# Kernel optimization log

Measured on AMD Instinct MI355X. Metric: run time of the kernel, lower is better.

Reference implementation:

```python
import jax, jax.numpy as jnp
import numpy as np
from jax import lax

IMG = 512            # image H = W
FH = FW = 32         # feature map spatial size
A = 9                # anchors per location (3 sizes x 3 ratios)
N = FH * FW * A      # total anchors = 9216
IOU_THR = 0.7
MIN_SCORE = 0.5
MIN_SIZE = 1e-3


def make_anchors():
    """Anchors in centroid format (cx, cy, w, h), ordered (H, W, A)."""
    stride = IMG / FH
    sizes = np.array([32.0, 64.0, 128.0])
    ratios = np.array([0.5, 1.0, 2.0])
    ws = (sizes[:, None] / np.sqrt(ratios)[None, :]).reshape(-1)  # (A,)
    hs = (sizes[:, None] * np.sqrt(ratios)[None, :]).reshape(-1)  # (A,)
    cx = (np.arange(FW) + 0.5) * stride
    cy = (np.arange(FH) + 0.5) * stride
    CX = np.broadcast_to(cx[None, :, None], (FH, FW, A))
    CY = np.broadcast_to(cy[:, None, None], (FH, FW, A))
    Wg = np.broadcast_to(ws[None, None, :], (FH, FW, A))
    Hg = np.broadcast_to(hs[None, None, :], (FH, FW, A))
    anc = np.stack([CX, CY, Wg, Hg], axis=-1).reshape(-1, 4)
    return jnp.asarray(anc, dtype=jnp.float32)


def pairwise_iou(b):
    # b: (N,4) corners x1,y1,x2,y2
    x1, y1, x2, y2 = b[:, 0], b[:, 1], b[:, 2], b[:, 3]
    area = (x2 - x1) * (y2 - y1)
    ix1 = jnp.maximum(x1[:, None], x1[None, :])
    iy1 = jnp.maximum(y1[:, None], y1[None, :])
    ix2 = jnp.minimum(x2[:, None], x2[None, :])
    iy2 = jnp.minimum(y2[:, None], y2[None, :])
    inter = jnp.maximum(ix2 - ix1, 0.0) * jnp.maximum(iy2 - iy1, 0.0)
    union = area[:, None] + area[None, :] - inter
    return inter / jnp.maximum(union, 1e-9)


def nms_keep(boxes, scores, valid):
    """Greedy NMS. Returns bool keep mask of shape (N,). Index decisions only."""
    s = jnp.where(valid, scores, -jnp.inf)
    order = jnp.argsort(-s)
    b = boxes[order]
    v = valid[order]
    ious = pairwise_iou(b)  # (N, N)
    idx = jnp.arange(N)

    def body(i, supp):
        keep_i = (~supp[i]) & v[i]
        return supp | (keep_i & (ious[i] > IOU_THR) & (idx > i))

    supp = lax.fori_loop(0, N, body, jnp.zeros(N, dtype=bool))
    keep_sorted = (~supp) & v
    return jnp.zeros(N, dtype=bool).at[order].set(keep_sorted)


def setup_inputs() -> dict:
    key = jax.random.key(0)
    ks = jax.random.split(key, 4)
    return {
        "feature_map": jax.random.normal(ks[0], (1, 256, FH, FW), jnp.float32),
        "conv1_w": jax.random.normal(ks[1], (512, 256, 3, 3), jnp.float32) * 0.02,
        "conv1_b": jnp.zeros((512,), jnp.float32),
        "conv2_w": jax.random.normal(ks[2], (A, 512), jnp.float32) * 0.01,
        "conv2_b": jnp.zeros((A,), jnp.float32),
        "conv3_w": jax.random.normal(ks[3], (4 * A, 512), jnp.float32) * 0.01,
        "conv3_b": jnp.zeros((4 * A,), jnp.float32),
    }


def reference(feature_map, conv1_w, conv1_b, conv2_w, conv2_b, conv3_w, conv3_b):
    anchors = make_anchors()  # (N,4) cx,cy,w,h

    # --- conv backbone head ---
    h = lax.conv_general_dilated(
        feature_map, conv1_w, (1, 1), "SAME",
        dimension_numbers=("NCHW", "OIHW", "NCHW"))
    h = jax.nn.relu(h + conv1_b[None, :, None, None])  # (1,512,H,W)

    scores = jax.nn.sigmoid(
        jnp.einsum("bchw,ac->bahw", h, conv2_w) + conv2_b[None, :, None, None])
    scores = scores.transpose(0, 2, 3, 1).reshape(-1)  # (N,) ordered (H,W,A)

    off = jnp.einsum("bchw,oc->bohw", h, conv3_w) + conv3_b[None, :, None, None]
    off = off.reshape(1, A, 4, FH, FW).transpose(0, 3, 4, 1, 2).reshape(-1, 4)

    acx, acy, aw, ah = anchors[:, 0], anchors[:, 1], anchors[:, 2], anchors[:, 3]
    cx = acx + off[:, 0] * aw
    cy = acy + off[:, 1] * ah
    bw = aw * jnp.exp(off[:, 2])
    bh = ah * jnp.exp(off[:, 3])
    boxes = jnp.stack([cx - bw / 2, cy - bh / 2, cx + bw / 2, cy + bh / 2], axis=1)

    # --- clip to image ---
    lo = jnp.array([0.0, 0.0, 0.0, 0.0], jnp.float32)
    hi = jnp.array([IMG, IMG, IMG, IMG], jnp.float32)
    boxes = jnp.clip(boxes, lo, hi)

    # --- remove small boxes + score threshold (as a mask, jit-safe) ---
    valid = ((boxes[:, 2] - boxes[:, 0]) >= MIN_SIZE) \
          & ((boxes[:, 3] - boxes[:, 1]) >= MIN_SIZE) \
          & (scores >= MIN_SCORE)

    # --- NMS (selection is index-based; no gradient through the decision) ---
    keep = nms_keep(lax.stop_gradient(boxes), lax.stop_gradient(scores), valid)

    out = jnp.concatenate(
        [boxes * keep[:, None].astype(boxes.dtype),
         (scores * keep.astype(scores.dtype))[:, None]], axis=1)  # (N,5)
    return out
```

## Files before the change

kernel.cpp:

```cpp
#include <hip/hip_runtime.h>
#include <math.h>

#define FHW   32
#define NA    9
#define NBOX  9216
#define C1    256
#define C2    512
#define KTOT  2304
#define KS    8
#define KCH   (KTOT / KS)
#define BK    16
#define NT    (KCH / BK)
#define CAP   64
#define ECAP  32768

struct AnchorWH { float w[NA]; float h[NA]; };

#define FP_OFF    0u
#define WT_OFF    1183744u
#define HP_OFF    5902336u
#define BOX_OFF   22679552u
#define SC_OFF    22827008u
#define VL_OFF    22863872u
#define DEG_OFF   22900736u
#define ADJ_OFF   22937600u
#define NV_OFF    24117248u

__global__ __launch_bounds__(256) void k_prep(const float* __restrict__ fin,
                                              float* __restrict__ Fp,
                                              unsigned int* __restrict__ deg,
                                              unsigned int* __restrict__ nv,
                                              const float* __restrict__ w1,
                                              float* __restrict__ Wt,
                                              float* __restrict__ out) {
    if (blockIdx.x < 1156) {
        int idx = blockIdx.x * 256 + threadIdx.x;
        if (idx < 256 * 34 * 34) {
            int c   = idx / 1156;
            int rem = idx - c * 1156;
            int yy  = rem / 34;
            int xx  = rem - yy * 34;
            float v = 0.f;
            if (yy >= 1 && yy <= 32 && xx >= 1 && xx <= 32)
                v = fin[c * 1024 + (yy - 1) * 32 + (xx - 1)];
            Fp[idx] = v;
        }
        if (idx < NBOX)     deg[idx] = 0u;
        if (idx < NBOX * 5) out[idx] = 0.f;
        if (idx == 0)       *nv = 0u;
    } else {
        __shared__ float tile[32][33];
        int tb  = blockIdx.x - 1156;
        int k0  = (tb % 72) * 32;
        int oc0 = (tb / 72) * 32;
        int t   = threadIdx.x;
        int r0 = t >> 5, c = t & 31;
        #pragma unroll
        for (int i = 0; i < 4; ++i) {
            int r = r0 + 8 * i;
            tile[r][c] = w1[(oc0 + r) * KTOT + k0 + c];
        }
        __syncthreads();
        #pragma unroll
        for (int i = 0; i < 4; ++i) {
            int kk  = r0 + 8 * i;
            int k   = k0 + kk;
            int ch  = k / 9;
            int kap = k - ch * 9;
            Wt[(kap * 256 + ch) * C2 + oc0 + c] = tile[c][kk];
        }
    }
}

__global__ __launch_bounds__(256) void k_gemm(const float* __restrict__ Fp,
                                              const float* __restrict__ Wt,
                                              float* __restrict__ hp) {
    const int id = blockIdx.x;
    const int kz = id & 7;
    const int g  = id >> 3;
    const int by = g & 3, bx = g >> 2;
    const int p0  = bx * 128;
    const int oc0 = by * 128;
    const int k0b = kz * KCH;
    const int t  = threadIdx.x;
    const int ty = t >> 4, tx = t & 15;

    __shared__ float As[BK][128];
    __shared__ float Bs[BK][128];

    const int pp  = t & 127;
    const int th  = t >> 7;
    const int pyx = ((p0 + pp) >> 5) * 34 + ((p0 + pp) & 31);
    const int rB  = t >> 5;
    const int cB  = (t & 31) * 4;

    float acc[2][2][4][4];
    #pragma unroll
    for (int rh = 0; rh < 2; ++rh)
        #pragma unroll
        for (int ch = 0; ch < 2; ++ch)
            #pragma unroll
            for (int r = 0; r < 4; ++r)
                #pragma unroll
                for (int c = 0; c < 4; ++c) acc[rh][ch][r][c] = 0.f;

    float  aS[8];
    float4 bS0, bS1;

    auto LOAD = [&](int s) {
        int tap = s >> 8, c0 = s & 255;
        int dy  = (tap * 11) >> 5;
        int dx  = tap - 3 * dy;
        const float* ab = Fp + ((c0 + th) * 34 + dy) * 34 + dx + pyx;
        #pragma unroll
        for (int i = 0; i < 8; ++i) aS[i] = ab[i * 2312];
        const float* bb = Wt + (s + rB) * C2 + oc0 + cB;
        bS0 = *(const float4*)bb;
        bS1 = *(const float4*)(bb + 8 * C2);
    };
    auto STORE = [&]() {
        #pragma unroll
        for (int i = 0; i < 8; ++i) As[2 * i + th][pp] = aS[i];
        *(float4*)&Bs[rB][cB]     = bS0;
        *(float4*)&Bs[rB + 8][cB] = bS1;
    };

    LOAD(k0b);
    #pragma unroll 1
    for (int tile = 0; tile < NT; ++tile) {
        __syncthreads();
        STORE();
        __syncthreads();
        if (tile + 1 < NT) LOAD(k0b + (tile + 1) * BK);
        #pragma unroll
        for (int kk = 0; kk < BK; ++kk) {
            float a[2][4], b[2][4];
            *(float4*)&a[0][0] = *(const float4*)&As[kk][ty * 4];
            *(float4*)&a[1][0] = *(const float4*)&As[kk][ty * 4 + 64];
            *(float4*)&b[0][0] = *(const float4*)&Bs[kk][tx * 4];
            *(float4*)&b[1][0] = *(const float4*)&Bs[kk][tx * 4 + 64];
            #pragma unroll
            for (int rh = 0; rh < 2; ++rh)
                #pragma unroll
                for (int ch = 0; ch < 2; ++ch)
                    #pragma unroll
                    for (int r = 0; r < 4; ++r)
                        #pragma unroll
                        for (int c = 0; c < 4; ++c)
                            acc[rh][ch][r][c] = fmaf(a[rh][r], b[ch][c], acc[rh][ch][r][c]);
        }
    }

    #pragma unroll
    for (int rh = 0; rh < 2; ++rh)
        #pragma unroll
        for (int r = 0; r < 4; ++r) {
            int p = p0 + rh * 64 + ty * 4 + r;
            float* dst = hp + ((size_t)(kz * 1024 + p)) * C2 + oc0 + tx * 4;
            *(float4*)dst        = *(float4*)&acc[rh][0][r][0];
            *(float4*)(dst + 64) = *(float4*)&acc[rh][1][r][0];
        }
}

__global__ __launch_bounds__(256) void k_heads(const float* __restrict__ hp,
                                               const float* __restrict__ b1,
                                               const float* __restrict__ w2,
                                               const float* __restrict__ b2,
                                               const float* __restrict__ w3,
                                               const float* __restrict__ b3,
                                               float* __restrict__ boxes,
                                               float* __restrict__ scoresG,
                                               unsigned int* __restrict__ nv,
                                               unsigned int* __restrict__ vlist,
                                               AnchorWH awh) {
    const int p0 = blockIdx.x * 4;
    const int t  = threadIdx.x;
    __shared__ float hrow[4][C2];
    __shared__ float arr[4][45];

    #pragma unroll
    for (int px = 0; px < 4; ++px) {
        int p = p0 + px;
        #pragma unroll
        for (int i = 0; i < 2; ++i) {
            int c = t + 256 * i;
            float s = b1[c];
            #pragma unroll
            for (int ks = 0; ks < KS; ++ks) s += hp[((size_t)(ks * 1024 + p)) * C2 + c];
            hrow[px][c] = fmaxf(s, 0.f);
        }
    }
    __syncthreads();

    const int w = t >> 6, lane = t & 63;
    for (int job = w; job < 180; job += 4) {
        int px = job / 45, j = job - px * 45;
        const float* wp = (j < 9) ? (w2 + j * C2) : (w3 + (j - 9) * C2);
        float s = 0.f;
        #pragma unroll
        for (int i = 0; i < 8; ++i) s += hrow[px][lane + 64 * i] * wp[lane + 64 * i];
        #pragma unroll
        for (int d = 1; d < 64; d <<= 1) s += __shfl_xor(s, d, 64);
        if (lane == 0) arr[px][j] = s;
    }
    __syncthreads();

    if (t < 36) {
        int px = t / 9, a = t - px * 9;
        int p = p0 + px;
        float logit = arr[px][a] + b2[a];
        float score = 1.f / (1.f + expf(-logit));
        float o0 = arr[px][9 + a * 4 + 0] + b3[a * 4 + 0];
        float o1 = arr[px][9 + a * 4 + 1] + b3[a * 4 + 1];
        float o2 = arr[px][9 + a * 4 + 2] + b3[a * 4 + 2];
        float o3 = arr[px][9 + a * 4 + 3] + b3[a * 4 + 3];
        int y = p >> 5, x = p & 31;
        float ax = (x + 0.5f) * 16.f, ay = (y + 0.5f) * 16.f;
        float aw = awh.w[a], ah = awh.h[a];
        float cx = ax + o0 * aw;
        float cy = ay + o1 * ah;
        float bw = aw * expf(o2);
        float bh = ah * expf(o3);
        float x1 = fminf(fmaxf(cx - bw * 0.5f, 0.f), 512.f);
        float y1 = fminf(fmaxf(cy - bh * 0.5f, 0.f), 512.f);
        float x2 = fminf(fmaxf(cx + bw * 0.5f, 0.f), 512.f);
        float y2 = fminf(fmaxf(cy + bh * 0.5f, 0.f), 512.f);
        int n = p * 9 + a;
        float4 bx4; bx4.x = x1; bx4.y = y1; bx4.z = x2; bx4.w = y2;
        ((float4*)boxes)[n] = bx4;
        scoresG[n] = score;
        bool valid = (x2 - x1 >= 0.001f) && (y2 - y1 >= 0.001f) && (score >= 0.5f);
        if (valid) {
            unsigned int ci = atomicAdd(nv, 1u);
            vlist[ci] = (unsigned int)n;
        }
    }
}

__global__ __launch_bounds__(256) void k_adj(const unsigned int* __restrict__ nvp,
                                             const unsigned int* __restrict__ vlist,
                                             const float* __restrict__ boxes,
                                             const float* __restrict__ scoresG,
                                             unsigned int* __restrict__ deg,
                                             unsigned short* __restrict__ adj) {
    const int Nv = (int)*nvp;
    int b = blockIdx.x;
    int tv = (int)(sqrtf(2.f * b + 0.25f) - 0.5f);
    while ((tv + 1) * (tv + 2) / 2 <= b) tv++;
    while (tv * (tv + 1) / 2 > b) tv--;
    int tu = b - tv * (tv + 1) / 2;
    if (tv * 128 >= Nv) return;

    __shared__ float4 ub[128], vb[128];
    __shared__ float  us[128], vs[128];
    __shared__ int    uo[128], vo[128];
    int t = threadIdx.x;
    if (t < 128) {
        int gi = tu * 128 + t;
        if (gi < Nv) { int n = (int)vlist[gi]; ub[t] = ((const float4*)boxes)[n]; us[t] = scoresG[n]; uo[t] = n; }
        else us[t] = -1.f;
    } else {
        int tt = t - 128;
        int gj = tv * 128 + tt;
        if (gj < Nv) { int n = (int)vlist[gj]; vb[tt] = ((const float4*)boxes)[n]; vs[tt] = scoresG[n]; vo[tt] = n; }
        else vs[tt] = -1.f;
    }
    __syncthreads();

    for (int s = 0; s < 64; ++s) {
        int q  = t + 256 * s;
        int i  = q >> 7, jj = q & 127;
        if (tu == tv && i >= jj) continue;
        float su = us[i], sv = vs[jj];
        if (su < 0.f || sv < 0.f) continue;
        float4 bu = ub[i], bv = vb[jj];
        float au = (bu.z - bu.x) * (bu.w - bu.y);
        float av = (bv.z - bv.x) * (bv.w - bv.y);
        float ix1 = fmaxf(bu.x, bv.x), iy1 = fmaxf(bu.y, bv.y);
        float ix2 = fminf(bu.z, bv.z), iy2 = fminf(bu.w, bv.w);
        float inter = fmaxf(ix2 - ix1, 0.f) * fmaxf(iy2 - iy1, 0.f);
        float uni = au + av - inter;
        float iou = inter / fmaxf(uni, 1e-9f);
        if (iou > 0.7f) {
            int gi = tu * 128 + i, gj = tv * 128 + jj;
            bool uHigh = (su > sv) || (su == sv && uo[i] < vo[jj]);
            int lower = uHigh ? gj : gi;
            int upper = uHigh ? gi : gj;
            unsigned int slot = atomicAdd(&deg[lower], 1u);
            if (slot < CAP) adj[lower * CAP + slot] = (unsigned short)upper;
        }
    }
}

__global__ __launch_bounds__(512) void k_peel(const unsigned int* __restrict__ nvp,
                                              const unsigned int* __restrict__ vlist,
                                              const unsigned int* __restrict__ degG,
                                              const unsigned short* __restrict__ adjG,
                                              const float* __restrict__ boxes,
                                              const float* __restrict__ scoresG,
                                              float* __restrict__ out) {
    __shared__ unsigned short offL[NBOX + 2];
    __shared__ unsigned char  st[NBOX];
    __shared__ unsigned short csr[ECAP];
    __shared__ unsigned int   scratch[512];
    const int t  = threadIdx.x;
    const int Nv = (int)*nvp;
    const int chunk = (Nv + 511) / 512;
    const int i0 = t * chunk;
    const int i1 = (i0 + chunk < Nv) ? (i0 + chunk) : Nv;

    unsigned int lsum = 0;
    for (int i = i0; i < i1; ++i) {
        unsigned int d = degG[i];
        if (d > CAP) d = CAP;
        st[i] = (unsigned char)d;
        lsum += d;
    }
    scratch[t] = lsum;
    __syncthreads();
    for (int ofs = 1; ofs < 512; ofs <<= 1) {
        unsigned int v = (t >= ofs) ? scratch[t - ofs] : 0u;
        __syncthreads();
        scratch[t] += v;
        __syncthreads();
    }
    if (t == 511) {
        unsigned int tot = scratch[511];
        offL[Nv] = (unsigned short)(tot < ECAP ? tot : ECAP);
    }
    unsigned int amask = 0;
    {
        unsigned int off = scratch[t] - lsum;
        for (int i = i0; i < i1; ++i) {
            unsigned int o = (off < ECAP) ? off : ECAP;
            offL[i] = (unsigned short)o;
            int d = st[i];
            int ld = (int)ECAP - (int)o; if (ld > d) ld = d; if (ld < 0) ld = 0;
            for (int s = 0; s < ld; ++s)
                csr[o + s] = adjG[i * CAP + s];
            off += d;
            if (d == 0) st[i] = 1;
            else { st[i] = 0; amask |= 1u << (i - i0); }
        }
    }
    __syncthreads();

    {
        volatile unsigned char* vst = st;
        int guard = 0;
        while (__any(amask != 0u) && guard < 100000) {
            ++guard;
            bool prog = false;
            unsigned int m = amask;
            while (m) {
                int b = __ffs(m) - 1; m &= m - 1;
                int i = i0 + b;
                int o = offL[i], on = offL[i + 1];
                int d, ld;
                if (on < ECAP) { d = on - o; ld = d; }
                else {
                    unsigned int dg = degG[i]; d = (dg > CAP) ? CAP : (int)dg;
                    ld = (int)ECAP - o; if (ld < 0) ld = 0; if (ld > d) ld = d;
                }
                bool kseen = false, useen = false;
                for (int s = 0; s < d; ++s) {
                    int j = (s < ld) ? (int)csr[o + s] : (int)adjG[i * CAP + s];
                    unsigned char v = vst[j];
                    kseen |= (v == 1);
                    useen |= (v == 0);
                }
                if (kseen)       { vst[i] = 2; prog = true; amask &= ~(1u << b); }
                else if (!useen) { vst[i] = 1; prog = true; amask &= ~(1u << b); }
            }
            if (!__any(prog)) __builtin_amdgcn_s_sleep(2);
        }
    }
    __syncthreads();

    for (int i = i0; i < i1; ++i) {
        if (st[i] == 1) {
            int n = (int)vlist[i];
            float4 b = ((const float4*)boxes)[n];
            out[n * 5 + 0] = b.x;
            out[n * 5 + 1] = b.y;
            out[n * 5 + 2] = b.z;
            out[n * 5 + 3] = b.w;
            out[n * 5 + 4] = scoresG[n];
        }
    }
}

extern "C" void kernel_launch(void* const* d_in, const int* in_sizes, int n_in,
                              void* d_out, int out_size, void* d_ws, size_t ws_size,
                              hipStream_t stream) {
    const float* fin = (const float*)d_in[0];
    const float* w1  = (const float*)d_in[1];
    const float* b1  = (const float*)d_in[2];
    const float* w2  = (const float*)d_in[3];
    const float* b2  = (const float*)d_in[4];
    const float* w3  = (const float*)d_in[5];
    const float* b3  = (const float*)d_in[6];
    float* out = (float*)d_out;

    char* ws = (char*)d_ws;
    float*          Fp    = (float*)(ws + FP_OFF);
    float*          Wt    = (float*)(ws + WT_OFF);
    float*          hp    = (float*)(ws + HP_OFF);
    float*          boxes = (float*)(ws + BOX_OFF);
    float*          sc    = (float*)(ws + SC_OFF);
    unsigned int*   vlist = (unsigned int*)(ws + VL_OFF);
    unsigned int*   deg   = (unsigned int*)(ws + DEG_OFF);
    unsigned short* adj   = (unsigned short*)(ws + ADJ_OFF);
    unsigned int*   nv    = (unsigned int*)(ws + NV_OFF);

    AnchorWH awh;
    {
        const double sizes[3]  = {32.0, 64.0, 128.0};
        const double ratios[3] = {0.5, 1.0, 2.0};
        for (int si = 0; si < 3; ++si)
            for (int ri = 0; ri < 3; ++ri) {
                awh.w[si * 3 + ri] = (float)(sizes[si] / sqrt(ratios[ri]));
                awh.h[si * 3 + ri] = (float)(sizes[si] * sqrt(ratios[ri]));
            }
    }

    k_prep<<<dim3(1156 + 72 * 16), 256, 0, stream>>>(fin, Fp, deg, nv, w1, Wt, out);
    k_gemm<<<dim3(256), 256, 0, stream>>>(Fp, Wt, hp);
    k_heads<<<dim3(256), 256, 0, stream>>>(hp, b1, w2, b2, w3, b3, boxes, sc, nv, vlist, awh);
    k_adj<<<dim3(72 * 73 / 2), 256, 0, stream>>>(nv, vlist, boxes, sc, deg, adj);
    k_peel<<<dim3(1), 512, 0, stream>>>(nv, vlist, deg, adj, boxes, sc, out);
}
```

Baseline: 204.0 us.

## Replace NMS peel neighbor scanning with push-based counter propagation

Graph construction now stores edges from each higher-scoring box to the boxes it can suppress, and packs an in-degree count alongside the out-degree. The peel kernel tracks, per box, the number of undecided higher-scoring neighbours plus a kept-neighbour count in one shared word. When a box is decided it pushes atomic updates to the boxes below it, so a waiting box only checks its own word instead of rescanning its neighbour list each round. This removes the prefix scan and the shared CSR copy. In exchange it adds an extra global atomic per edge during graph build, shared atomics during peeling, and an idle-based exit in place of the iteration guard.

```diff
diff --git a/kernel.cpp b/kernel.cpp
--- a/kernel.cpp
+++ b/kernel.cpp
@@ -12,7 +12,7 @@
 #define BK    16
 #define NT    (KCH / BK)
 #define CAP   64
-#define ECAP  32768
+#define CAPL  4
 
 struct AnchorWH { float w[NA]; float h[NA]; };
 
@@ -284,10 +284,13 @@
         if (iou > 0.7f) {
             int gi = tu * 128 + i, gj = tv * 128 + jj;
             bool uHigh = (su > sv) || (su == sv && uo[i] < vo[jj]);
-            int lower = uHigh ? gj : gi;
-            int upper = uHigh ? gi : gj;
-            unsigned int slot = atomicAdd(&deg[lower], 1u);
-            if (slot < CAP) adj[lower * CAP + slot] = (unsigned short)upper;
+            int hi = uHigh ? gi : gj;
+            int lo = uHigh ? gj : gi;
+            unsigned int old = atomicAdd(&deg[hi], 1u);
+            if ((old & 0xFFFFu) < CAP) {
+                adj[hi * CAP + (old & 0xFFFFu)] = (unsigned short)lo;
+                atomicAdd(&deg[lo], 0x10000u);
+            }
         }
     }
 }
@@ -299,80 +302,74 @@
                                               const float* __restrict__ boxes,
                                               const float* __restrict__ scoresG,
                                               float* __restrict__ out) {
-    __shared__ unsigned short offL[NBOX + 2];
+    __shared__ unsigned int   word[NBOX];
     __shared__ unsigned char  st[NBOX];
-    __shared__ unsigned short csr[ECAP];
-    __shared__ unsigned int   scratch[512];
+    __shared__ unsigned short outL[NBOX * CAPL];
     const int t  = threadIdx.x;
     const int Nv = (int)*nvp;
     const int chunk = (Nv + 511) / 512;
     const int i0 = t * chunk;
     const int i1 = (i0 + chunk < Nv) ? (i0 + chunk) : Nv;
 
-    unsigned int lsum = 0;
+    unsigned int amask = 0, smask = 0;
     for (int i = i0; i < i1; ++i) {
-        unsigned int d = degG[i];
-        if (d > CAP) d = CAP;
-        st[i] = (unsigned char)d;
-        lsum += d;
-    }
-    scratch[t] = lsum;
+        unsigned int dg = degG[i];
+        int cin  = (int)(dg >> 16);
+        int dout = (int)(dg & 0xFFFFu); if (dout > CAP) dout = CAP;
+        int dl = (dout < CAPL) ? dout : CAPL;
+        for (int s = 0; s < dl; ++s)
+            outL[i * CAPL + s] = adjG[i * CAP + s];
+        word[i] = (unsigned int)cin;
+        st[i] = 0;
+        if (cin == 0) smask |= 1u << (i - i0);
+        else          amask |= 1u << (i - i0);
+    }
     __syncthreads();
-    for (int ofs = 1; ofs < 512; ofs <<= 1) {
-        unsigned int v = (t >= ofs) ? scratch[t - ofs] : 0u;
-        __syncthreads();
-        scratch[t] += v;
-        __syncthreads();
-    }
-    if (t == 511) {
-        unsigned int tot = scratch[511];
-        offL[Nv] = (unsigned short)(tot < ECAP ? tot : ECAP);
-    }
-    unsigned int amask = 0;
+
+    auto PUSH = [&](int i, bool kept) {
+        unsigned int dg = degG[i];
+        int dout = (int)(dg & 0xFFFFu); if (dout > CAP) dout = CAP;
+        unsigned int delta = kept ? 0xFFFFu : 0xFFFFFFFFu;
+        for (int s = 0; s < dout; ++s) {
+            int j = (s < CAPL) ? (int)outL[i * CAPL + s]
+                               : (int)adjG[i * CAP + s];
+            atomicAdd(&word[j], delta);
+        }
+    };
+
     {
-        unsigned int off = scratch[t] - lsum;
-        for (int i = i0; i < i1; ++i) {
-            unsigned int o = (off < ECAP) ? off : ECAP;
-            offL[i] = (unsigned short)o;
-            int d = st[i];
-            int ld = (int)ECAP - (int)o; if (ld > d) ld = d; if (ld < 0) ld = 0;
-            for (int s = 0; s < ld; ++s)
-                csr[o + s] = adjG[i * CAP + s];
-            off += d;
-            if (d == 0) st[i] = 1;
-            else { st[i] = 0; amask |= 1u << (i - i0); }
-        }
-    }
-    __syncthreads();
+        unsigned int m = smask;
+        while (m) {
+            int b = __ffs(m) - 1; m &= m - 1;
+            int i = i0 + b;
+            st[i] = 1;
+            PUSH(i, true);
+        }
+    }
 
     {
-        volatile unsigned char* vst = st;
-        int guard = 0;
-        while (__any(amask != 0u) && guard < 100000) {
-            ++guard;
+        volatile unsigned int* vw = word;
+        int idle = 0;
+        while (__any(amask != 0u)) {
             bool prog = false;
             unsigned int m = amask;
             while (m) {
                 int b = __ffs(m) - 1; m &= m - 1;
                 int i = i0 + b;
-                int o = offL[i], on = offL[i + 1];
-                int d, ld;
-                if (on < ECAP) { d = on - o; ld = d; }
-                else {
-                    unsigned int dg = degG[i]; d = (dg > CAP) ? CAP : (int)dg;
-                    ld = (int)ECAP - o; if (ld < 0) ld = 0; if (ld > d) ld = d;
+                unsigned int w = vw[i];
+                if ((w & 0xFFFFu) == 0u) {
+                    bool kept = (w >> 16) == 0u;
+                    st[i] = kept ? 1 : 2;
+                    PUSH(i, kept);
+                    amask &= ~(1u << b);
+                    prog = true;
                 }
-                bool kseen = false, useen = false;
-                for (int s = 0; s < d; ++s) {
-                    int j = (s < ld) ? (int)csr[o + s] : (int)adjG[i * CAP + s];
-                    unsigned char v = vst[j];
-                    kseen |= (v == 1);
-                    useen |= (v == 0);
-                }
-                if (kseen)       { vst[i] = 2; prog = true; amask &= ~(1u << b); }
-                else if (!useen) { vst[i] = 1; prog = true; amask &= ~(1u << b); }
             }
-            if (!__any(prog)) __builtin_amdgcn_s_sleep(2);
+            if (__any(prog)) idle = 0;
+            else {
+                if (++idle > 8000) break;
+                __builtin_amdgcn_s_sleep(1);
+            }
         }
     }
     __syncthreads();
```

New measurement: 194.0 us. 1.05x faster.
